# Kernel tuning notes

Hardware: AMD Instinct MI355X
Metric: run time of the kernel (lower is better)

## Reference

```python
import jax, jax.numpy as jnp
import numpy as np

N = 100000   # nodes
E = 1600000  # edges (before self-loops)
D_IN = 128
HID = 64
H1 = 4       # heads of conv1
OUT = 2
EPS = 1e-5
NEG_SLOPE = 0.2


def setup_inputs():
    key = jax.random.key(0)
    ks = jax.random.split(key, 12)
    s = 0.1
    return {
        "x": jax.random.normal(ks[0], (N, D_IN), jnp.float32),
        "edge_index": jax.random.randint(ks[1], (2, E), 0, N, jnp.int64),
        "W1": jax.random.normal(ks[2], (D_IN, H1 * HID), jnp.float32) * s,
        "att_src1": jax.random.normal(ks[3], (H1, HID), jnp.float32) * s,
        "att_dst1": jax.random.normal(ks[4], (H1, HID), jnp.float32) * s,
        "b1": jnp.zeros((H1 * HID,), jnp.float32),
        "g1": jnp.ones((H1 * HID,), jnp.float32),
        "be1": jnp.zeros((H1 * HID,), jnp.float32),
        "W2": jax.random.normal(ks[5], (H1 * HID, HID), jnp.float32) * s,
        "att_src2": jax.random.normal(ks[6], (1, HID), jnp.float32) * s,
        "att_dst2": jax.random.normal(ks[7], (1, HID), jnp.float32) * s,
        "b2": jnp.zeros((HID,), jnp.float32),
        "g2": jnp.ones((HID,), jnp.float32),
        "be2": jnp.zeros((HID,), jnp.float32),
        "Wc1": jax.random.normal(ks[8], (HID, HID // 2), jnp.float32) * s,
        "bc1": jnp.zeros((HID // 2,), jnp.float32),
        "Wc2": jax.random.normal(ks[9], (HID // 2, OUT), jnp.float32) * s,
        "bc2": jnp.zeros((OUT,), jnp.float32),
    }


def _gat(x, W, a_src, a_dst, bias, src, dst, heads):
    n = x.shape[0]
    h = (x @ W).reshape(n, heads, -1)              # [N,H,C]
    e_src = jnp.einsum('nhc,hc->nh', h, a_src)     # [N,H]
    e_dst = jnp.einsum('nhc,hc->nh', h, a_dst)
    e = jax.nn.leaky_relu(e_src[src] + e_dst[dst], NEG_SLOPE)  # [Etot,H]
    m = jax.ops.segment_max(e, dst, num_segments=n)            # edge-softmax over incoming
    p = jnp.exp(e - m[dst])
    z = jax.ops.segment_sum(p, dst, num_segments=n)
    alpha = p / z[dst]
    msg = alpha[:, :, None] * h[src]               # [Etot,H,C]
    out = jax.ops.segment_sum(msg, dst, num_segments=n)        # [N,H,C]
    return out.reshape(n, -1) + bias               # concat heads + bias


def _bn(x, g, b):
    m = x.mean(0)
    v = x.var(0)
    return g * (x - m) * jax.lax.rsqrt(v + EPS) + b


def reference(x, edge_index, W1, att_src1, att_dst1, b1, g1, be1,
              W2, att_src2, att_dst2, b2, g2, be2, Wc1, bc1, Wc2, bc2):
    n = x.shape[0]
    loops = jnp.arange(n, dtype=edge_index.dtype)
    src = jnp.concatenate([edge_index[0], loops])  # PyG add_self_loops=True
    dst = jnp.concatenate([edge_index[1], loops])

    h = _gat(x, W1, att_src1, att_dst1, b1, src, dst, H1)
    h = jax.nn.elu(_bn(h, g1, be1))                # dropout = identity (eval)
    h = _gat(h, W2, att_src2, att_dst2, b2, src, dst, 1)
    h = jax.nn.elu(_bn(h, g2, be2))
    h = jax.nn.elu(h @ Wc1 + bc1)
    logits = h @ Wc2 + bc2
    return jax.nn.log_softmax(logits, axis=1)
```

## Files before the change

kernel.cpp:

```cpp
#include <hip/hip_runtime.h>
#include <hip/hip_bf16.h>

constexpr int N_  = 100000;
constexpr int E_  = 1600000;
constexpr int PAD = 48;
constexpr int NBKT = 196;
constexpr int BCAP = 16384;

constexpr size_t P_PARAMS = 12288;
constexpr size_t OFF_WPK1 = 224000;
constexpr size_t OFF_WPK2 = 289536;
constexpr size_t OFF_DEG  = 322304;
constexpr size_t OFF_ES1  = 722304;
constexpr size_t OFF_ED1  = 2322304;
constexpr size_t OFF_ES2  = 3922304;
constexpr size_t OFF_ED2  = 4322304;
constexpr size_t OFF_CSR  = 4722304;
constexpr size_t OFF_H1   = 23922304;
constexpr size_t OFF_H2   = OFF_H1;
constexpr size_t OFF_AGG2 = OFF_H1 + 12800000;
constexpr size_t OFF_AGG1 = 75122304;
constexpr size_t OFF_BKT  = 126322304;

typedef unsigned short ushortT;
typedef short bf16x8 __attribute__((ext_vector_type(8)));
typedef float f32x4 __attribute__((ext_vector_type(4)));

#define DEV __device__ __forceinline__

DEV float leakyf(float x) { return x > 0.f ? x : 0.2f * x; }
DEV float eluf(float x)   { return x > 0.f ? x : __expf(x) - 1.f; }
DEV float rbf(unsigned short u) { unsigned int b = ((unsigned int)u) << 16; return __uint_as_float(b); }
DEV unsigned short f2b(float f) { __hip_bfloat16 h = __float2bfloat16(f); return *reinterpret_cast<unsigned short*>(&h); }
DEV float sel_head(float4 a, int hd) {
    float r = a.x;
    r = (hd == 1) ? a.y : r;
    r = (hd == 2) ? a.z : r;
    r = (hd == 3) ? a.w : r;
    return r;
}
DEV unsigned short sel_h4(ushort4 u, int hd) {
    unsigned short r = u.x;
    r = (hd == 1) ? u.y : r;
    r = (hd == 2) ? u.z : r;
    r = (hd == 3) ? u.w : r;
    return r;
}
DEV int eread(const int* __restrict__ ei, int mode, int idx) {
    return mode ? ei[(size_t)idx * 2] : ei[idx];
}

__global__ void k_detect2(const int* __restrict__ ei, const unsigned int* __restrict__ g1raw,
                          int* __restrict__ mode, int* __restrict__ fmode) {
    __shared__ int any;
    if (threadIdx.x == 0) any = 0;
    __syncthreads();
    if (ei[2 * threadIdx.x + 1] != 0) atomicOr(&any, 1);
    __syncthreads();
    if (threadIdx.x == 0) {
        *mode = any ? 0 : 1;
        *fmode = (g1raw[0] == 0x3F800000u) ? 0 : 1;
    }
}

struct CvtArgs { const void* src[16]; int off[17]; };
__global__ __launch_bounds__(256) void k_cvtall(CvtArgs a, float* __restrict__ dst,
                                                const int* __restrict__ fmode, int total) {
    int i = blockIdx.x * 256 + threadIdx.x;
    if (i >= total) return;
    int seg = 0;
    #pragma unroll
    for (int s2 = 1; s2 < 16; ++s2) seg += (i >= a.off[s2]);
    int j = i - a.off[seg];
    float v;
    if (*fmode) v = rbf(((const unsigned short*)a.src[seg])[j]);
    else        v = ((const float*)a.src[seg])[j];
    dst[i] = v;
}

__global__ __launch_bounds__(256) void k_packw(const float* __restrict__ pp,
                                               ushortT* __restrict__ w1, ushortT* __restrict__ w2) {
    int i = blockIdx.x * 256 + threadIdx.x;
    if (i < 32768) {
        int j = i & 7, lane = (i >> 3) & 63, ks = (i >> 9) & 3, ct = i >> 11;
        int src = (ks * 32 + ((lane >> 4) << 3) + j) * 256 + ct * 16 + (lane & 15);
        w1[i] = f2b(pp[src]);
    } else if (i < 49152) {
        int i2 = i - 32768;
        int j = i2 & 7, lane = (i2 >> 3) & 63, ks = (i2 >> 9) & 7, ct = i2 >> 12;
        int src = (ks * 32 + ((lane >> 4) << 3) + j) * 64 + ct * 16 + (lane & 15);
        w2[i2] = f2b(pp[34048 + src]);
    }
}

__global__ __launch_bounds__(256) void k_bin(const int* __restrict__ ei, const int* __restrict__ mode,
                                             unsigned int* __restrict__ bucketArr,
                                             int* __restrict__ bucketCursor) {
    __shared__ unsigned int pk[8192];
    __shared__ int cnt[256], scn[256], bse[256], cur[256], gb[256];
    int tid = threadIdx.x;
    cnt[tid] = 0;
    __syncthreads();
    int e0 = blockIdx.x * 8192;
    int m = *mode;
    #pragma unroll 4
    for (int j = 0; j < 32; ++j) {
        int e = e0 + j * 256 + tid;
        if (e < E_) atomicAdd(&cnt[eread(ei, m, E_ + e) >> 9], 1);
    }
    __syncthreads();
    int v = cnt[tid];
    scn[tid] = v;
    __syncthreads();
    for (int d = 1; d < 256; d <<= 1) {
        int t2 = (tid >= d) ? scn[tid - d] : 0;
        __syncthreads();
        scn[tid] += t2;
        __syncthreads();
    }
    int excl = scn[tid] - v;
    bse[tid] = excl;
    cur[tid] = excl;
    __syncthreads();
    #pragma unroll 4
    for (int j = 0; j < 32; ++j) {
        int e = e0 + j * 256 + tid;
        if (e < E_) {
            int s = eread(ei, m, e);
            int d = eread(ei, m, E_ + e);
            int b = d >> 9;
            int p = atomicAdd(&cur[b], 1);
            pk[p] = ((unsigned int)(d & 511) << 17) | (unsigned int)s;
        }
    }
    __syncthreads();
    if (tid < NBKT) {
        int c = cnt[tid];
        gb[tid] = (c > 0) ? atomicAdd(&bucketCursor[tid], c) : 0;
    }
    __syncthreads();
    int wv = tid >> 6, ln = tid & 63;
    for (int b = wv; b < NBKT; b += 4) {
        int c = cnt[b];
        int lo = bse[b], g = gb[b];
        for (int i = ln; i < c; i += 64) {
            int gi = g + i;
            if (gi < BCAP) bucketArr[(size_t)b * BCAP + gi] = pk[lo + i];
        }
    }
}

__global__ __launch_bounds__(256) void k_csr(const unsigned int* __restrict__ bucketArr,
                                             const int* __restrict__ bucketCursor,
                                             int* __restrict__ csr, int* __restrict__ deg) {
    __shared__ int dl[512];
    int tid = threadIdx.x;
    int b = blockIdx.x;
    int nbase = b * 512;
    int nb = min(N_ - nbase, 512);
    if (nb <= 0) return;
    dl[tid] = 0; dl[tid + 256] = 0;
    __syncthreads();
    int c = min(bucketCursor[b], BCAP);
    const unsigned int* run = bucketArr + (size_t)b * BCAP;
    for (int i = tid; i < c; i += 256) {
        unsigned int p = run[i];
        int s = (int)(p & 0x1FFFFu);
        int dloc = (int)(p >> 17);
        int slot = atomicAdd(&dl[dloc], 1);
        if (slot < PAD - 1) csr[(size_t)(nbase + dloc) * PAD + slot] = s;
    }
    __syncthreads();
    for (int t = tid; t < nb; t += 256) {
        int n = nbase + t;
        int cd = min(dl[t], PAD - 1);
        csr[(size_t)n * PAD + cd] = n;
        deg[n] = cd + 1;
    }
}

__global__ __launch_bounds__(256) void k_gemm1f(const void* __restrict__ x, const int* __restrict__ fmode,
                                                const ushortT* __restrict__ wpk,
                                                const float* __restrict__ as1, const float* __restrict__ ad1,
                                                ushortT* __restrict__ h1,
                                                float* __restrict__ es1, float* __restrict__ ed1) {
    __shared__ ushortT xs[32][132];
    int tid = threadIdx.x, w = tid >> 6, lane = tid & 63;
    int l15 = lane & 15, l4 = lane >> 4;
    int row0 = blockIdx.x * 32;
    if (*fmode) {
        const ushortT* xg = (const ushortT*)x + (size_t)row0 * 128;
        for (int i = tid; i < 512; i += 256) {
            int r = i >> 4, cc = (i & 15) * 8;
            ushort4 a = *(const ushort4*)(xg + r * 128 + cc);
            ushort4 b = *(const ushort4*)(xg + r * 128 + cc + 4);
            *(ushort4*)&xs[r][cc]     = a;
            *(ushort4*)&xs[r][cc + 4] = b;
        }
    } else {
        const float* xg = (const float*)x + (size_t)row0 * 128;
        for (int i = tid; i < 512; i += 256) {
            int r = i >> 4, cc = (i & 15) * 8;
            float4 a = *(const float4*)(xg + r * 128 + cc);
            float4 b = *(const float4*)(xg + r * 128 + cc + 4);
            *(ushort4*)&xs[r][cc]     = make_ushort4(f2b(a.x), f2b(a.y), f2b(a.z), f2b(a.w));
            *(ushort4*)&xs[r][cc + 4] = make_ushort4(f2b(b.x), f2b(b.y), f2b(b.z), f2b(b.w));
        }
    }
    __syncthreads();
    bf16x8 A[2][4];
    #pragma unroll
    for (int rt = 0; rt < 2; ++rt)
        #pragma unroll
        for (int ks = 0; ks < 4; ++ks)
            A[rt][ks] = *(const bf16x8*)&xs[rt * 16 + l15][ks * 32 + l4 * 8];
    f32x4 acc[2][4];
    #pragma unroll
    for (int rt = 0; rt < 2; ++rt)
        #pragma unroll
        for (int ct = 0; ct < 4; ++ct) acc[rt][ct] = (f32x4){0.f, 0.f, 0.f, 0.f};
    const bf16x8* wp = (const bf16x8*)wpk;
    #pragma unroll
    for (int ct = 0; ct < 4; ++ct) {
        int ctg = w * 4 + ct;
        bf16x8 B0 = wp[(ctg * 4 + 0) * 64 + lane];
        bf16x8 B1 = wp[(ctg * 4 + 1) * 64 + lane];
        bf16x8 B2 = wp[(ctg * 4 + 2) * 64 + lane];
        bf16x8 B3 = wp[(ctg * 4 + 3) * 64 + lane];
        #pragma unroll
        for (int rt = 0; rt < 2; ++rt) {
            acc[rt][ct] = __builtin_amdgcn_mfma_f32_16x16x32_bf16(A[rt][0], B0, acc[rt][ct], 0, 0, 0);
            acc[rt][ct] = __builtin_amdgcn_mfma_f32_16x16x32_bf16(A[rt][1], B1, acc[rt][ct], 0, 0, 0);
            acc[rt][ct] = __builtin_amdgcn_mfma_f32_16x16x32_bf16(A[rt][2], B2, acc[rt][ct], 0, 0, 0);
            acc[rt][ct] = __builtin_amdgcn_mfma_f32_16x16x32_bf16(A[rt][3], B3, acc[rt][ct], 0, 0, 0);
        }
    }
    float asc[4], adc[4];
    #pragma unroll
    for (int ct = 0; ct < 4; ++ct) {
        asc[ct] = as1[w * 64 + ct * 16 + l15];
        adc[ct] = ad1[w * 64 + ct * 16 + l15];
    }
    float pes[2][4], ped[2][4];
    #pragma unroll
    for (int rt = 0; rt < 2; ++rt)
        #pragma unroll
        for (int r = 0; r < 4; ++r) { pes[rt][r] = 0.f; ped[rt][r] = 0.f; }
    #pragma unroll
    for (int rt = 0; rt < 2; ++rt)
        #pragma unroll
        for (int ct = 0; ct < 4; ++ct)
            #pragma unroll
            for (int r = 0; r < 4; ++r) {
                float v = acc[rt][ct][r];
                int row = row0 + rt * 16 + l4 * 4 + r;
                h1[(size_t)row * 256 + w * 64 + ct * 16 + l15] = f2b(v);
                pes[rt][r] = fmaf(v, asc[ct], pes[rt][r]);
                ped[rt][r] = fmaf(v, adc[ct], ped[rt][r]);
            }
    #pragma unroll
    for (int d = 1; d < 16; d <<= 1)
        #pragma unroll
        for (int rt = 0; rt < 2; ++rt)
            #pragma unroll
            for (int r = 0; r < 4; ++r) {
                pes[rt][r] += __shfl_xor(pes[rt][r], d);
                ped[rt][r] += __shfl_xor(ped[rt][r], d);
            }
    if (l15 == 0) {
        #pragma unroll
        for (int rt = 0; rt < 2; ++rt)
            #pragma unroll
            for (int r = 0; r < 4; ++r) {
                int row = row0 + rt * 16 + l4 * 4 + r;
                es1[row * 4 + w] = pes[rt][r];
                ed1[row * 4 + w] = ped[rt][r];
            }
    }
}

__global__ __launch_bounds__(256) void k_lagg1(const ushortT* __restrict__ h1,
                                               const float* __restrict__ es1, const float* __restrict__ ed1,
                                               const int* __restrict__ deg, const int* __restrict__ csr,
                                               const float* __restrict__ b1, ushortT* __restrict__ out) {
    __shared__ int ssrc[4][PAD];
    __shared__ ushort4 sp[4][PAD];
    int wid = threadIdx.x >> 6;
    int lane = threadIdx.x & 63;
    int n = blockIdx.x * 4 + wid;
    int cnt = deg[n];
    int start = n * PAD;
    float4 ed = ((const float4*)ed1)[n];
    float z0 = 0.f, z1 = 0.f, z2 = 0.f, z3 = 0.f;
    if (lane < cnt) {
        int s = csr[start + lane];
        ssrc[wid][lane] = s;
        float4 es = ((const float4*)es1)[s];
        float p0 = __expf(leakyf(es.x + ed.x));
        float p1 = __expf(leakyf(es.y + ed.y));
        float p2 = __expf(leakyf(es.z + ed.z));
        float p3 = __expf(leakyf(es.w + ed.w));
        sp[wid][lane] = make_ushort4(f2b(p0), f2b(p1), f2b(p2), f2b(p3));
        z0 = p0; z1 = p1; z2 = p2; z3 = p3;
    }
    #pragma unroll
    for (int d = 1; d < 64; d <<= 1) {
        z0 += __shfl_xor(z0, d); z1 += __shfl_xor(z1, d);
        z2 += __shfl_xor(z2, d); z3 += __shfl_xor(z3, d);
    }
    int half = lane >> 5, lh = lane & 31, hd = lh >> 3;
    float izh = sel_head(make_float4(1.f / z0, 1.f / z1, 1.f / z2, 1.f / z3), hd);
    float a0 = 0.f, a1 = 0.f, a2 = 0.f, a3 = 0.f, a4 = 0.f, a5 = 0.f, a6 = 0.f, a7 = 0.f;
    float c0 = 0.f, c1 = 0.f, c2 = 0.f, c3 = 0.f, c4 = 0.f, c5 = 0.f, c6 = 0.f, c7 = 0.f;
    int iters = (cnt + 1) >> 1;
    for (int t = 0; t < iters; t += 4) {
        int i0 = 2 * t + half;
        int i1 = i0 + 2, i2 = i0 + 4, i3 = i0 + 6;
        bool v0 = i0 < cnt, v1 = i1 < cnt, v2 = i2 < cnt, v3 = i3 < cnt;
        int s0 = ssrc[wid][v0 ? i0 : 0];
        int s1 = ssrc[wid][v1 ? i1 : 0];
        int s2 = ssrc[wid][v2 ? i2 : 0];
        int s3 = ssrc[wid][v3 ? i3 : 0];
        ushort4 u0 = sp[wid][v0 ? i0 : 0];
        ushort4 u1 = sp[wid][v1 ? i1 : 0];
        ushort4 u2 = sp[wid][v2 ? i2 : 0];
        ushort4 u3 = sp[wid][v3 ? i3 : 0];
        float w0 = v0 ? rbf(sel_h4(u0, hd)) * izh : 0.f;
        float w1 = v1 ? rbf(sel_h4(u1, hd)) * izh : 0.f;
        float w2 = v2 ? rbf(sel_h4(u2, hd)) * izh : 0.f;
        float w3 = v3 ? rbf(sel_h4(u3, hd)) * izh : 0.f;
        uint4 r0 = *(const uint4*)(h1 + (size_t)s0 * 256 + lh * 8);
        uint4 r1 = *(const uint4*)(h1 + (size_t)s1 * 256 + lh * 8);
        uint4 r2 = *(const uint4*)(h1 + (size_t)s2 * 256 + lh * 8);
        uint4 r3 = *(const uint4*)(h1 + (size_t)s3 * 256 + lh * 8);
        a0 = fmaf(w0, rbf((unsigned short)(r0.x & 0xffff)), a0);
        a1 = fmaf(w0, rbf((unsigned short)(r0.x >> 16)), a1);
        a2 = fmaf(w0, rbf((unsigned short)(r0.y & 0xffff)), a2);
        a3 = fmaf(w0, rbf((unsigned short)(r0.y >> 16)), a3);
        a4 = fmaf(w0, rbf((unsigned short)(r0.z & 0xffff)), a4);
        a5 = fmaf(w0, rbf((unsigned short)(r0.z >> 16)), a5);
        a6 = fmaf(w0, rbf((unsigned short)(r0.w & 0xffff)), a6);
        a7 = fmaf(w0, rbf((unsigned short)(r0.w >> 16)), a7);
        c0 = fmaf(w1, rbf((unsigned short)(r1.x & 0xffff)), c0);
        c1 = fmaf(w1, rbf((unsigned short)(r1.x >> 16)), c1);
        c2 = fmaf(w1, rbf((unsigned short)(r1.y & 0xffff)), c2);
        c3 = fmaf(w1, rbf((unsigned short)(r1.y >> 16)), c3);
        c4 = fmaf(w1, rbf((unsigned short)(r1.z & 0xffff)), c4);
        c5 = fmaf(w1, rbf((unsigned short)(r1.z >> 16)), c5);
        c6 = fmaf(w1, rbf((unsigned short)(r1.w & 0xffff)), c6);
        c7 = fmaf(w1, rbf((unsigned short)(r1.w >> 16)), c7);
        a0 = fmaf(w2, rbf((unsigned short)(r2.x & 0xffff)), a0);
        a1 = fmaf(w2, rbf((unsigned short)(r2.x >> 16)), a1);
        a2 = fmaf(w2, rbf((unsigned short)(r2.y & 0xffff)), a2);
        a3 = fmaf(w2, rbf((unsigned short)(r2.y >> 16)), a3);
        a4 = fmaf(w2, rbf((unsigned short)(r2.z & 0xffff)), a4);
        a5 = fmaf(w2, rbf((unsigned short)(r2.z >> 16)), a5);
        a6 = fmaf(w2, rbf((unsigned short)(r2.w & 0xffff)), a6);
        a7 = fmaf(w2, rbf((unsigned short)(r2.w >> 16)), a7);
        c0 = fmaf(w3, rbf((unsigned short)(r3.x & 0xffff)), c0);
        c1 = fmaf(w3, rbf((unsigned short)(r3.x >> 16)), c1);
        c2 = fmaf(w3, rbf((unsigned short)(r3.y & 0xffff)), c2);
        c3 = fmaf(w3, rbf((unsigned short)(r3.y >> 16)), c3);
        c4 = fmaf(w3, rbf((unsigned short)(r3.z & 0xffff)), c4);
        c5 = fmaf(w3, rbf((unsigned short)(r3.z >> 16)), c5);
        c6 = fmaf(w3, rbf((unsigned short)(r3.w & 0xffff)), c6);
        c7 = fmaf(w3, rbf((unsigned short)(r3.w >> 16)), c7);
    }
    a0 += c0; a1 += c1; a2 += c2; a3 += c3; a4 += c4; a5 += c5; a6 += c6; a7 += c7;
    a0 += __shfl_xor(a0, 32); a1 += __shfl_xor(a1, 32);
    a2 += __shfl_xor(a2, 32); a3 += __shfl_xor(a3, 32);
    a4 += __shfl_xor(a4, 32); a5 += __shfl_xor(a5, 32);
    a6 += __shfl_xor(a6, 32); a7 += __shfl_xor(a7, 32);
    if (half == 0) {
        float4 b0 = *(const float4*)(b1 + lh * 8);
        float4 b1v = *(const float4*)(b1 + lh * 8 + 4);
        ushort4 o0 = make_ushort4(f2b(a0 + b0.x), f2b(a1 + b0.y), f2b(a2 + b0.z), f2b(a3 + b0.w));
        ushort4 o1 = make_ushort4(f2b(a4 + b1v.x), f2b(a5 + b1v.y), f2b(a6 + b1v.z), f2b(a7 + b1v.w));
        *(ushort4*)(out + (size_t)n * 256 + lh * 8)     = o0;
        *(ushort4*)(out + (size_t)n * 256 + lh * 8 + 4) = o1;
    }
}

__global__ __launch_bounds__(256) void k_bnstats1(const ushortT* __restrict__ a, double* __restrict__ sums,
                                                  double* __restrict__ sumsq) {
    int c = threadIdx.x;
    int r0 = blockIdx.x * 256;
    int r1 = min(r0 + 256, N_);
    double s = 0.0, q = 0.0;
    for (int r = r0; r < r1; ++r) { float v = rbf(a[(size_t)r * 256 + c]); s += v; q += (double)v * v; }
    atomicAdd(&sums[c], s);
    atomicAdd(&sumsq[c], q);
}

__global__ void k_bnfin(const double* __restrict__ sums, const double* __restrict__ sumsq,
                        const float* __restrict__ g, const float* __restrict__ be,
                        float* __restrict__ s, float* __restrict__ t, int C) {
    int c = threadIdx.x;
    if (c < C) {
        double mean = sums[c] / (double)N_;
        double var = fmax(sumsq[c] / (double)N_ - mean * mean, 0.0);
        double sc = (double)g[c] / sqrt(var + 1e-5);
        s[c] = (float)sc;
        t[c] = (float)((double)be[c] - mean * sc);
    }
}

__global__ __launch_bounds__(256) void k_gemm2f(const ushortT* __restrict__ agg1,
                                                const ushortT* __restrict__ wpk2,
                                                const float* __restrict__ sc1, const float* __restrict__ tc1,
                                                const float* __restrict__ as2, const float* __restrict__ ad2,
                                                ushortT* __restrict__ h2,
                                                float* __restrict__ es2, float* __restrict__ ed2) {
    int tid = threadIdx.x, w = tid >> 6, lane = tid & 63;
    int l15 = lane & 15, l4 = lane >> 4;
    int row0 = blockIdx.x * 64;
    int arow = row0 + w * 16 + l15;
    int ar = min(arow, N_ - 1);
    bf16x8 A[8];
    #pragma unroll
    for (int ks = 0; ks < 8; ++ks) {
        const ushortT* ap = agg1 + (size_t)ar * 256 + ks * 32 + l4 * 8;
        int pi = ks * 32 + l4 * 8;
        uint4 u = *(const uint4*)ap;
        float4 s0 = *(const float4*)(sc1 + pi);
        float4 s1 = *(const float4*)(sc1 + pi + 4);
        float4 t0 = *(const float4*)(tc1 + pi);
        float4 t1 = *(const float4*)(tc1 + pi + 4);
        float e0 = eluf(fmaf(rbf((unsigned short)(u.x & 0xffff)), s0.x, t0.x));
        float e1 = eluf(fmaf(rbf((unsigned short)(u.x >> 16)),    s0.y, t0.y));
        float e2 = eluf(fmaf(rbf((unsigned short)(u.y & 0xffff)), s0.z, t0.z));
        float e3 = eluf(fmaf(rbf((unsigned short)(u.y >> 16)),    s0.w, t0.w));
        float e4 = eluf(fmaf(rbf((unsigned short)(u.z & 0xffff)), s1.x, t1.x));
        float e5 = eluf(fmaf(rbf((unsigned short)(u.z >> 16)),    s1.y, t1.y));
        float e6 = eluf(fmaf(rbf((unsigned short)(u.w & 0xffff)), s1.z, t1.z));
        float e7 = eluf(fmaf(rbf((unsigned short)(u.w >> 16)),    s1.w, t1.w));
        A[ks] = (bf16x8){(short)f2b(e0), (short)f2b(e1), (short)f2b(e2), (short)f2b(e3),
                         (short)f2b(e4), (short)f2b(e5), (short)f2b(e6), (short)f2b(e7)};
    }
    f32x4 acc[4];
    #pragma unroll
    for (int ct = 0; ct < 4; ++ct) acc[ct] = (f32x4){0.f, 0.f, 0.f, 0.f};
    const bf16x8* wp = (const bf16x8*)wpk2;
    #pragma unroll
    for (int ct = 0; ct < 4; ++ct) {
        #pragma unroll
        for (int ks = 0; ks < 8; ++ks) {
            bf16x8 B = wp[(ct * 8 + ks) * 64 + lane];
            acc[ct] = __builtin_amdgcn_mfma_f32_16x16x32_bf16(A[ks], B, acc[ct], 0, 0, 0);
        }
    }
    float asc[4], adc[4];
    #pragma unroll
    for (int ct = 0; ct < 4; ++ct) {
        asc[ct] = as2[ct * 16 + l15];
        adc[ct] = ad2[ct * 16 + l15];
    }
    float pes[4] = {0.f, 0.f, 0.f, 0.f}, ped[4] = {0.f, 0.f, 0.f, 0.f};
    #pragma unroll
    for (int ct = 0; ct < 4; ++ct)
        #pragma unroll
        for (int r = 0; r < 4; ++r) {
            float v = acc[ct][r];
            int row = row0 + w * 16 + l4 * 4 + r;
            if (row < N_) h2[(size_t)row * 64 + ct * 16 + l15] = f2b(v);
            pes[r] = fmaf(v, asc[ct], pes[r]);
            ped[r] = fmaf(v, adc[ct], ped[r]);
        }
    #pragma unroll
    for (int d = 1; d < 16; d <<= 1)
        #pragma unroll
        for (int r = 0; r < 4; ++r) {
            pes[r] += __shfl_xor(pes[r], d);
            ped[r] += __shfl_xor(ped[r], d);
        }
    if (l15 == 0) {
        #pragma unroll
        for (int r = 0; r < 4; ++r) {
            int row = row0 + w * 16 + l4 * 4 + r;
            if (row < N_) { es2[row] = pes[r]; ed2[row] = ped[r]; }
        }
    }
}

__global__ __launch_bounds__(256) void k_lagg2(const ushortT* __restrict__ h2,
                                               const float* __restrict__ es2, const float* __restrict__ ed2,
                                               const int* __restrict__ deg, const int* __restrict__ csr,
                                               const float* __restrict__ b2, float* __restrict__ out) {
    __shared__ int ssrc[4][PAD];
    __shared__ float sp[4][PAD];
    int wid = threadIdx.x >> 6;
    int lane = threadIdx.x & 63;
    int n = blockIdx.x * 4 + wid;
    int cnt = deg[n];
    int start = n * PAD;
    float ed = ed2[n];
    float z = 0.f;
    if (lane < cnt) {
        int s = csr[start + lane];
        ssrc[wid][lane] = s;
        float p = __expf(leakyf(es2[s] + ed));
        sp[wid][lane] = p;
        z = p;
    }
    #pragma unroll
    for (int d = 1; d < 64; d <<= 1) z += __shfl_xor(z, d);
    float iz = 1.f / z;
    int half = lane >> 5, lh = lane & 31;
    float a0 = 0.f, a1 = 0.f, c0 = 0.f, c1 = 0.f;
    int iters = (cnt + 1) >> 1;
    for (int t = 0; t < iters; t += 4) {
        int i0 = 2 * t + half;
        int i1 = i0 + 2, i2 = i0 + 4, i3 = i0 + 6;
        bool v0 = i0 < cnt, v1 = i1 < cnt, v2 = i2 < cnt, v3 = i3 < cnt;
        int s0 = ssrc[wid][v0 ? i0 : 0];
        int s1 = ssrc[wid][v1 ? i1 : 0];
        int s2 = ssrc[wid][v2 ? i2 : 0];
        int s3 = ssrc[wid][v3 ? i3 : 0];
        float w0 = v0 ? sp[wid][i0] * iz : 0.f;
        float w1 = v1 ? sp[wid][i1] * iz : 0.f;
        float w2 = v2 ? sp[wid][i2] * iz : 0.f;
        float w3 = v3 ? sp[wid][i3] * iz : 0.f;
        unsigned int u0 = *(const unsigned int*)(h2 + (size_t)s0 * 64 + lh * 2);
        unsigned int u1 = *(const unsigned int*)(h2 + (size_t)s1 * 64 + lh * 2);
        unsigned int u2 = *(const unsigned int*)(h2 + (size_t)s2 * 64 + lh * 2);
        unsigned int u3 = *(const unsigned int*)(h2 + (size_t)s3 * 64 + lh * 2);
        a0 = fmaf(w0, rbf((unsigned short)(u0 & 0xffff)), a0);
        a1 = fmaf(w0, rbf((unsigned short)(u0 >> 16)), a1);
        c0 = fmaf(w1, rbf((unsigned short)(u1 & 0xffff)), c0);
        c1 = fmaf(w1, rbf((unsigned short)(u1 >> 16)), c1);
        a0 = fmaf(w2, rbf((unsigned short)(u2 & 0xffff)), a0);
        a1 = fmaf(w2, rbf((unsigned short)(u2 >> 16)), a1);
        c0 = fmaf(w3, rbf((unsigned short)(u3 & 0xffff)), c0);
        c1 = fmaf(w3, rbf((unsigned short)(u3 >> 16)), c1);
    }
    a0 += c0; a1 += c1;
    a0 += __shfl_xor(a0, 32);
    a1 += __shfl_xor(a1, 32);
    if (half == 0) {
        out[(size_t)n * 64 + lh * 2 + 0] = a0 + b2[lh * 2 + 0];
        out[(size_t)n * 64 + lh * 2 + 1] = a1 + b2[lh * 2 + 1];
    }
}

__global__ __launch_bounds__(256) void k_bnstats2(const float* __restrict__ a, double* __restrict__ sums,
                                                  double* __restrict__ sumsq) {
    __shared__ double sm[256], sq[256];
    int tid = threadIdx.x;
    int c = tid & 63, rr = tid >> 6;
    int r0 = blockIdx.x * 1024;
    int r1 = min(r0 + 1024, N_);
    double s = 0.0, q = 0.0;
    for (int r = r0 + rr; r < r1; r += 4) { float v = a[(size_t)r * 64 + c]; s += v; q += (double)v * v; }
    sm[tid] = s; sq[tid] = q; __syncthreads();
    if (tid < 64) {
        s = sm[tid] + sm[tid + 64] + sm[tid + 128] + sm[tid + 192];
        q = sq[tid] + sq[tid + 64] + sq[tid + 128] + sq[tid + 192];
        atomicAdd(&sums[tid], s);
        atomicAdd(&sumsq[tid], q);
    }
}

__global__ __launch_bounds__(256) void k_cls(const float* __restrict__ agg2, const float* __restrict__ Wc1,
                                             const float* __restrict__ bc1, const float* __restrict__ Wc2,
                                             const float* __restrict__ bc2, const float* __restrict__ s2,
                                             const float* __restrict__ t2, float* __restrict__ out) {
    __shared__ float w1s[2048];
    __shared__ float w2s[64];
    __shared__ float b1s[32];
    __shared__ float b2s[2];
    __shared__ float ss[64], ts[64];
    int tid = threadIdx.x;
    for (int i = tid; i < 2048; i += 256) w1s[i] = Wc1[i];
    if (tid < 64) { w2s[tid] = Wc2[tid]; ss[tid] = s2[tid]; ts[tid] = t2[tid]; }
    if (tid < 32) b1s[tid] = bc1[tid];
    if (tid < 2)  b2s[tid] = bc2[tid];
    __syncthreads();
    int n = blockIdx.x * 256 + tid;
    if (n >= N_) return;
    float hv[64];
    const float4* rp = (const float4*)(agg2 + (size_t)n * 64);
    #pragma unroll
    for (int q = 0; q < 16; ++q) {
        float4 v = rp[q];
        float tmp[4] = {v.x, v.y, v.z, v.w};
        #pragma unroll
        for (int c4 = 0; c4 < 4; ++c4) {
            int c = q * 4 + c4;
            hv[c] = eluf(fmaf(tmp[c4], ss[c], ts[c]));
        }
    }
    float l0 = b2s[0], l1 = b2s[1];
    for (int j = 0; j < 32; ++j) {
        float a = b1s[j];
        #pragma unroll
        for (int k = 0; k < 64; ++k) a = fmaf(hv[k], w1s[k * 32 + j], a);
        float u = eluf(a);
        l0 = fmaf(u, w2s[j * 2 + 0], l0);
        l1 = fmaf(u, w2s[j * 2 + 1], l1);
    }
    float mx = fmaxf(l0, l1);
    float lse = mx + __logf(__expf(l0 - mx) + __expf(l1 - mx));
    out[(size_t)n * 2 + 0] = l0 - lse;
    out[(size_t)n * 2 + 1] = l1 - lse;
}

extern "C" void kernel_launch(void* const* d_in, const int* in_sizes, int n_in,
                              void* d_out, int out_size, void* d_ws, size_t ws_size,
                              hipStream_t stream) {
    float* out = (float*)d_out;

    char* ws = (char*)d_ws;
    double* sums1  = (double*)(ws + 0);
    double* sumsq1 = (double*)(ws + 2048);
    double* sums2  = (double*)(ws + 4096);
    double* sumsq2 = (double*)(ws + 4608);
    int* bcur = (int*)(ws + 5120);
    float* s1 = (float*)(ws + 6144), *t1 = (float*)(ws + 7168);
    float* s2 = (float*)(ws + 8192), *t2 = (float*)(ws + 8448);
    int* mode  = (int*)(ws + 8704);
    int* fmode = (int*)(ws + 8708);

    float* pp   = (float*)(ws + P_PARAMS);
    float* as1f = pp + 32768;
    float* ad1f = pp + 33024;
    float* b1f  = pp + 33280;
    float* g1f  = pp + 33536;
    float* be1f = pp + 33792;
    float* as2f = pp + 50432;
    float* ad2f = pp + 50496;
    float* b2f  = pp + 50560;
    float* g2f  = pp + 50624;
    float* be2f = pp + 50688;
    float* Wc1f = pp + 50752;
    float* bc1f = pp + 52800;
    float* Wc2f = pp + 52832;
    float* bc2f = pp + 52896;
    const int CV_TOTAL = 52898;

    ushortT* wpk1 = (ushortT*)(ws + OFF_WPK1);
    ushortT* wpk2 = (ushortT*)(ws + OFF_WPK2);
    int* deg    = (int*)(ws + OFF_DEG);
    int* csr    = (int*)(ws + OFF_CSR);
    float* es1  = (float*)(ws + OFF_ES1);
    float* ed1  = (float*)(ws + OFF_ED1);
    float* es2  = (float*)(ws + OFF_ES2);
    float* ed2  = (float*)(ws + OFF_ED2);
    ushortT* h1 = (ushortT*)(ws + OFF_H1);
    ushortT* h2 = (ushortT*)(ws + OFF_H2);
    float* agg2 = (float*)(ws + OFF_AGG2);
    ushortT* agg1 = (ushortT*)(ws + OFF_AGG1);
    unsigned int* bkt = (unsigned int*)(ws + OFF_BKT);

    hipMemsetAsync(ws, 0, 6144, stream);
    k_detect2<<<1, 256, 0, stream>>>((const int*)d_in[1], (const unsigned int*)d_in[6], mode, fmode);

    CvtArgs ca;
    const int srcIdx[16] = {2,3,4,5,6,7,8,9,10,11,12,13,14,15,16,17};
    const int offsEl[17] = {0,32768,33024,33280,33536,33792,34048,50432,50496,50560,
                            50624,50688,50752,52800,52832,52896,52898};
    for (int i = 0; i < 16; ++i) ca.src[i] = d_in[srcIdx[i]];
    for (int i = 0; i < 17; ++i) ca.off[i] = offsEl[i];
    k_cvtall<<<(CV_TOTAL + 255) / 256, 256, 0, stream>>>(ca, pp, fmode, CV_TOTAL);
    k_packw <<<192, 256, 0, stream>>>(pp, wpk1, wpk2);

    k_bin<<<(E_ + 8191) / 8192, 256, 0, stream>>>((const int*)d_in[1], mode, bkt, bcur);
    k_csr<<<NBKT, 256, 0, stream>>>(bkt, bcur, csr, deg);

    k_gemm1f<<<N_ / 32, 256, 0, stream>>>(d_in[0], fmode, wpk1, as1f, ad1f, h1, es1, ed1);
    k_lagg1<<<N_ / 4, 256, 0, stream>>>(h1, es1, ed1, deg, csr, b1f, agg1);
    k_bnstats1<<<(N_ + 255) / 256, 256, 0, stream>>>(agg1, sums1, sumsq1);
    k_bnfin<<<1, 256, 0, stream>>>(sums1, sumsq1, g1f, be1f, s1, t1, 256);

    k_gemm2f<<<(N_ + 63) / 64, 256, 0, stream>>>(agg1, wpk2, s1, t1, as2f, ad2f, h2, es2, ed2);
    k_lagg2<<<N_ / 4, 256, 0, stream>>>(h2, es2, ed2, deg, csr, b2f, agg2);
    k_bnstats2<<<98, 256, 0, stream>>>(agg2, sums2, sumsq2);
    k_bnfin<<<1, 64, 0, stream>>>(sums2, sumsq2, g2f, be2f, s2, t2, 64);

    k_cls<<<(N_ + 255) / 256, 256, 0, stream>>>(agg2, Wc1f, bc1f, Wc2f, bc2f, s2, t2, out);
}
```

Baseline: 473.3 us.

## Fuse setup kernels, cache edges in LDS, unroll gathers, vectorize BN stats

Merges the detect, convert and weight-pack setup kernels into one kernel that reads raw weights directly, and folds the edge-format detection into the binning kernel. k_bin now keeps src/dst in shared memory so it does not reread edges from global memory. Both aggregation loops issue eight gathers before doing the FMAs, giving more memory-level parallelism. BN stats for layer 1 use 16-byte loads, float partial sums and a shared-memory reduction. The risks are more LDS per bin block, which lowers occupancy, and float rather than double accumulation inside each block.

```diff
diff --git a/kernel.cpp b/kernel.cpp
--- a/kernel.cpp
+++ b/kernel.cpp
@@ -7,20 +7,24 @@
 constexpr int NBKT = 196;
 constexpr int BCAP = 16384;
 
-constexpr size_t P_PARAMS = 12288;
-constexpr size_t OFF_WPK1 = 224000;
-constexpr size_t OFF_WPK2 = 289536;
-constexpr size_t OFF_DEG  = 322304;
-constexpr size_t OFF_ES1  = 722304;
-constexpr size_t OFF_ED1  = 2322304;
-constexpr size_t OFF_ES2  = 3922304;
-constexpr size_t OFF_ED2  = 4322304;
-constexpr size_t OFF_CSR  = 4722304;
-constexpr size_t OFF_H1   = 23922304;
+constexpr size_t P_PARAMS = 8192;
+constexpr size_t OFF_S1   = 24576;
+constexpr size_t OFF_T1   = 25600;
+constexpr size_t OFF_S2   = 26624;
+constexpr size_t OFF_T2   = 26880;
+constexpr size_t OFF_WPK1 = 27136;
+constexpr size_t OFF_WPK2 = 92672;
+constexpr size_t OFF_DEG  = 125696;
+constexpr size_t OFF_ES1  = 525696;
+constexpr size_t OFF_ED1  = 2125696;
+constexpr size_t OFF_ES2  = 3725696;
+constexpr size_t OFF_ED2  = 4125696;
+constexpr size_t OFF_CSR  = 4525696;
+constexpr size_t OFF_H1   = 23725696;
 constexpr size_t OFF_H2   = OFF_H1;
 constexpr size_t OFF_AGG2 = OFF_H1 + 12800000;
-constexpr size_t OFF_AGG1 = 75122304;
-constexpr size_t OFF_BKT  = 126322304;
+constexpr size_t OFF_AGG1 = 74925696;
+constexpr size_t OFF_BKT  = 126125696;
 
 typedef unsigned short ushortT;
 typedef short bf16x8 __attribute__((ext_vector_type(8)));
@@ -49,64 +53,66 @@
 DEV int eread(const int* __restrict__ ei, int mode, int idx) {
     return mode ? ei[(size_t)idx * 2] : ei[idx];
 }
-
-__global__ void k_detect2(const int* __restrict__ ei, const unsigned int* __restrict__ g1raw,
-                          int* __restrict__ mode, int* __restrict__ fmode) {
-    __shared__ int any;
-    if (threadIdx.x == 0) any = 0;
-    __syncthreads();
-    if (ei[2 * threadIdx.x + 1] != 0) atomicOr(&any, 1);
-    __syncthreads();
-    if (threadIdx.x == 0) {
-        *mode = any ? 0 : 1;
-        *fmode = (g1raw[0] == 0x3F800000u) ? 0 : 1;
-    }
-}
-
-struct CvtArgs { const void* src[16]; int off[17]; };
-__global__ __launch_bounds__(256) void k_cvtall(CvtArgs a, float* __restrict__ dst,
-                                                const int* __restrict__ fmode, int total) {
+DEV unsigned short praw(const void* p, int fm, int idx) {
+    return fm ? ((const ushortT*)p)[idx] : f2b(((const float*)p)[idx]);
+}
+
+struct CvtArgs { const void* src[14]; int off[15]; };
+__global__ __launch_bounds__(256) void k_setup(const void* __restrict__ W1raw, const void* __restrict__ W2raw,
+                                               const unsigned int* __restrict__ g1raw, CvtArgs ca,
+                                               ushortT* __restrict__ w1, ushortT* __restrict__ w2,
+                                               float* __restrict__ pp) {
     int i = blockIdx.x * 256 + threadIdx.x;
-    if (i >= total) return;
-    int seg = 0;
-    #pragma unroll
-    for (int s2 = 1; s2 < 16; ++s2) seg += (i >= a.off[s2]);
-    int j = i - a.off[seg];
-    float v;
-    if (*fmode) v = rbf(((const unsigned short*)a.src[seg])[j]);
-    else        v = ((const float*)a.src[seg])[j];
-    dst[i] = v;
-}
-
-__global__ __launch_bounds__(256) void k_packw(const float* __restrict__ pp,
-                                               ushortT* __restrict__ w1, ushortT* __restrict__ w2) {
-    int i = blockIdx.x * 256 + threadIdx.x;
+    int fm = (g1raw[0] == 0x3F800000u) ? 0 : 1;
     if (i < 32768) {
         int j = i & 7, lane = (i >> 3) & 63, ks = (i >> 9) & 3, ct = i >> 11;
         int src = (ks * 32 + ((lane >> 4) << 3) + j) * 256 + ct * 16 + (lane & 15);
-        w1[i] = f2b(pp[src]);
+        w1[i] = praw(W1raw, fm, src);
     } else if (i < 49152) {
         int i2 = i - 32768;
         int j = i2 & 7, lane = (i2 >> 3) & 63, ks = (i2 >> 9) & 7, ct = i2 >> 12;
         int src = (ks * 32 + ((lane >> 4) << 3) + j) * 64 + ct * 16 + (lane & 15);
-        w2[i2] = f2b(pp[34048 + src]);
-    }
-}
-
-__global__ __launch_bounds__(256) void k_bin(const int* __restrict__ ei, const int* __restrict__ mode,
+        w2[i2] = praw(W2raw, fm, src);
+    } else if (i < 52898) {
+        int j = i - 49152;
+        int seg = 0;
+        #pragma unroll
+        for (int s2 = 1; s2 < 14; ++s2) seg += (j >= ca.off[s2]);
+        int k = j - ca.off[seg];
+        float v;
+        if (fm) v = rbf(((const ushortT*)ca.src[seg])[k]);
+        else    v = ((const float*)ca.src[seg])[k];
+        pp[j] = v;
+    }
+}
+
+__global__ __launch_bounds__(256) void k_bin(const int* __restrict__ ei,
                                              unsigned int* __restrict__ bucketArr,
                                              int* __restrict__ bucketCursor) {
     __shared__ unsigned int pk[8192];
+    __shared__ int sdl[8192];
+    __shared__ int ssl[8192];
     __shared__ int cnt[256], scn[256], bse[256], cur[256], gb[256];
+    __shared__ int any;
     int tid = threadIdx.x;
     cnt[tid] = 0;
-    __syncthreads();
+    if (tid == 0) any = 0;
+    __syncthreads();
+    if (ei[2 * tid + 1] != 0) atomicOr(&any, 1);
+    __syncthreads();
+    int m = any ? 0 : 1;
     int e0 = blockIdx.x * 8192;
-    int m = *mode;
     #pragma unroll 4
     for (int j = 0; j < 32; ++j) {
-        int e = e0 + j * 256 + tid;
-        if (e < E_) atomicAdd(&cnt[eread(ei, m, E_ + e) >> 9], 1);
+        int idx = j * 256 + tid;
+        int e = e0 + idx;
+        if (e < E_) {
+            int s = eread(ei, m, e);
+            int d = eread(ei, m, E_ + e);
+            ssl[idx] = s;
+            sdl[idx] = d;
+            atomicAdd(&cnt[d >> 9], 1);
+        }
     }
     __syncthreads();
     int v = cnt[tid];
@@ -124,10 +130,10 @@
     __syncthreads();
     #pragma unroll 4
     for (int j = 0; j < 32; ++j) {
-        int e = e0 + j * 256 + tid;
+        int idx = j * 256 + tid;
+        int e = e0 + idx;
         if (e < E_) {
-            int s = eread(ei, m, e);
-            int d = eread(ei, m, E_ + e);
+            int s = ssl[idx], d = sdl[idx];
             int b = d >> 9;
             int p = atomicAdd(&cur[b], 1);
             pk[p] = ((unsigned int)(d & 511) << 17) | (unsigned int)s;
@@ -179,7 +185,8 @@
     }
 }
 
-__global__ __launch_bounds__(256) void k_gemm1f(const void* __restrict__ x, const int* __restrict__ fmode,
+__global__ __launch_bounds__(256) void k_gemm1f(const void* __restrict__ x,
+                                                const unsigned int* __restrict__ g1raw,
                                                 const ushortT* __restrict__ wpk,
                                                 const float* __restrict__ as1, const float* __restrict__ ad1,
                                                 ushortT* __restrict__ h1,
@@ -188,7 +195,8 @@
     int tid = threadIdx.x, w = tid >> 6, lane = tid & 63;
     int l15 = lane & 15, l4 = lane >> 4;
     int row0 = blockIdx.x * 32;
-    if (*fmode) {
+    int fm = (g1raw[0] == 0x3F800000u) ? 0 : 1;
+    if (fm) {
         const ushortT* xg = (const ushortT*)x + (size_t)row0 * 128;
         for (int i = tid; i < 512; i += 256) {
             int r = i >> 4, cc = (i & 15) * 8;
@@ -313,58 +321,43 @@
     float a0 = 0.f, a1 = 0.f, a2 = 0.f, a3 = 0.f, a4 = 0.f, a5 = 0.f, a6 = 0.f, a7 = 0.f;
     float c0 = 0.f, c1 = 0.f, c2 = 0.f, c3 = 0.f, c4 = 0.f, c5 = 0.f, c6 = 0.f, c7 = 0.f;
     int iters = (cnt + 1) >> 1;
-    for (int t = 0; t < iters; t += 4) {
-        int i0 = 2 * t + half;
-        int i1 = i0 + 2, i2 = i0 + 4, i3 = i0 + 6;
-        bool v0 = i0 < cnt, v1 = i1 < cnt, v2 = i2 < cnt, v3 = i3 < cnt;
-        int s0 = ssrc[wid][v0 ? i0 : 0];
-        int s1 = ssrc[wid][v1 ? i1 : 0];
-        int s2 = ssrc[wid][v2 ? i2 : 0];
-        int s3 = ssrc[wid][v3 ? i3 : 0];
-        ushort4 u0 = sp[wid][v0 ? i0 : 0];
-        ushort4 u1 = sp[wid][v1 ? i1 : 0];
-        ushort4 u2 = sp[wid][v2 ? i2 : 0];
-        ushort4 u3 = sp[wid][v3 ? i3 : 0];
-        float w0 = v0 ? rbf(sel_h4(u0, hd)) * izh : 0.f;
-        float w1 = v1 ? rbf(sel_h4(u1, hd)) * izh : 0.f;
-        float w2 = v2 ? rbf(sel_h4(u2, hd)) * izh : 0.f;
-        float w3 = v3 ? rbf(sel_h4(u3, hd)) * izh : 0.f;
-        uint4 r0 = *(const uint4*)(h1 + (size_t)s0 * 256 + lh * 8);
-        uint4 r1 = *(const uint4*)(h1 + (size_t)s1 * 256 + lh * 8);
-        uint4 r2 = *(const uint4*)(h1 + (size_t)s2 * 256 + lh * 8);
-        uint4 r3 = *(const uint4*)(h1 + (size_t)s3 * 256 + lh * 8);
-        a0 = fmaf(w0, rbf((unsigned short)(r0.x & 0xffff)), a0);
-        a1 = fmaf(w0, rbf((unsigned short)(r0.x >> 16)), a1);
-        a2 = fmaf(w0, rbf((unsigned short)(r0.y & 0xffff)), a2);
-        a3 = fmaf(w0, rbf((unsigned short)(r0.y >> 16)), a3);
-        a4 = fmaf(w0, rbf((unsigned short)(r0.z & 0xffff)), a4);
-        a5 = fmaf(w0, rbf((unsigned short)(r0.z >> 16)), a5);
-        a6 = fmaf(w0, rbf((unsigned short)(r0.w & 0xffff)), a6);
-        a7 = fmaf(w0, rbf((unsigned short)(r0.w >> 16)), a7);
-        c0 = fmaf(w1, rbf((unsigned short)(r1.x & 0xffff)), c0);
-        c1 = fmaf(w1, rbf((unsigned short)(r1.x >> 16)), c1);
-        c2 = fmaf(w1, rbf((unsigned short)(r1.y & 0xffff)), c2);
-        c3 = fmaf(w1, rbf((unsigned short)(r1.y >> 16)), c3);
-        c4 = fmaf(w1, rbf((unsigned short)(r1.z & 0xffff)), c4);
-        c5 = fmaf(w1, rbf((unsigned short)(r1.z >> 16)), c5);
-        c6 = fmaf(w1, rbf((unsigned short)(r1.w & 0xffff)), c6);
-        c7 = fmaf(w1, rbf((unsigned short)(r1.w >> 16)), c7);
-        a0 = fmaf(w2, rbf((unsigned short)(r2.x & 0xffff)), a0);
-        a1 = fmaf(w2, rbf((unsigned short)(r2.x >> 16)), a1);
-        a2 = fmaf(w2, rbf((unsigned short)(r2.y & 0xffff)), a2);
-        a3 = fmaf(w2, rbf((unsigned short)(r2.y >> 16)), a3);
-        a4 = fmaf(w2, rbf((unsigned short)(r2.z & 0xffff)), a4);
-        a5 = fmaf(w2, rbf((unsigned short)(r2.z >> 16)), a5);
-        a6 = fmaf(w2, rbf((unsigned short)(r2.w & 0xffff)), a6);
-        a7 = fmaf(w2, rbf((unsigned short)(r2.w >> 16)), a7);
-        c0 = fmaf(w3, rbf((unsigned short)(r3.x & 0xffff)), c0);
-        c1 = fmaf(w3, rbf((unsigned short)(r3.x >> 16)), c1);
-        c2 = fmaf(w3, rbf((unsigned short)(r3.y & 0xffff)), c2);
-        c3 = fmaf(w3, rbf((unsigned short)(r3.y >> 16)), c3);
-        c4 = fmaf(w3, rbf((unsigned short)(r3.z & 0xffff)), c4);
-        c5 = fmaf(w3, rbf((unsigned short)(r3.z >> 16)), c5);
-        c6 = fmaf(w3, rbf((unsigned short)(r3.w & 0xffff)), c6);
-        c7 = fmaf(w3, rbf((unsigned short)(r3.w >> 16)), c7);
+    for (int t = 0; t < iters; t += 8) {
+        int sArr[8]; float wArr[8]; uint4 rArr[8];
+        #pragma unroll
+        for (int u = 0; u < 8; ++u) {
+            int i = 2 * (t + u) + half;
+            bool v = i < cnt;
+            sArr[u] = ssrc[wid][v ? i : 0];
+            ushort4 uu = sp[wid][v ? i : 0];
+            wArr[u] = v ? rbf(sel_h4(uu, hd)) * izh : 0.f;
+        }
+        #pragma unroll
+        for (int u = 0; u < 8; ++u)
+            rArr[u] = *(const uint4*)(h1 + (size_t)sArr[u] * 256 + lh * 8);
+        #pragma unroll
+        for (int u = 0; u < 8; ++u) {
+            float wv = wArr[u];
+            uint4 r = rArr[u];
+            if (u & 1) {
+                c0 = fmaf(wv, rbf((unsigned short)(r.x & 0xffff)), c0);
+                c1 = fmaf(wv, rbf((unsigned short)(r.x >> 16)), c1);
+                c2 = fmaf(wv, rbf((unsigned short)(r.y & 0xffff)), c2);
+                c3 = fmaf(wv, rbf((unsigned short)(r.y >> 16)), c3);
+                c4 = fmaf(wv, rbf((unsigned short)(r.z & 0xffff)), c4);
+                c5 = fmaf(wv, rbf((unsigned short)(r.z >> 16)), c5);
+                c6 = fmaf(wv, rbf((unsigned short)(r.w & 0xffff)), c6);
+                c7 = fmaf(wv, rbf((unsigned short)(r.w >> 16)), c7);
+            } else {
+                a0 = fmaf(wv, rbf((unsigned short)(r.x & 0xffff)), a0);
+                a1 = fmaf(wv, rbf((unsigned short)(r.x >> 16)), a1);
+                a2 = fmaf(wv, rbf((unsigned short)(r.y & 0xffff)), a2);
+                a3 = fmaf(wv, rbf((unsigned short)(r.y >> 16)), a3);
+                a4 = fmaf(wv, rbf((unsigned short)(r.z & 0xffff)), a4);
+                a5 = fmaf(wv, rbf((unsigned short)(r.z >> 16)), a5);
+                a6 = fmaf(wv, rbf((unsigned short)(r.w & 0xffff)), a6);
+                a7 = fmaf(wv, rbf((unsigned short)(r.w >> 16)), a7);
+            }
+        }
     }
     a0 += c0; a1 += c1; a2 += c2; a3 += c3; a4 += c4; a5 += c5; a6 += c6; a7 += c7;
     a0 += __shfl_xor(a0, 32); a1 += __shfl_xor(a1, 32);
@@ -383,13 +376,38 @@
 
 __global__ __launch_bounds__(256) void k_bnstats1(const ushortT* __restrict__ a, double* __restrict__ sums,
                                                   double* __restrict__ sumsq) {
-    int c = threadIdx.x;
-    int r0 = blockIdx.x * 256;
-    int r1 = min(r0 + 256, N_);
-    double s = 0.0, q = 0.0;
-    for (int r = r0; r < r1; ++r) { float v = rbf(a[(size_t)r * 256 + c]); s += v; q += (double)v * v; }
-    atomicAdd(&sums[c], s);
-    atomicAdd(&sumsq[c], q);
+    __shared__ float lss[256][9], lsq[256][9];
+    int tid = threadIdx.x;
+    int c8 = tid & 31, rr = tid >> 5;
+    int r0 = blockIdx.x * 512;
+    int r1 = min(r0 + 512, N_);
+    float s[8] = {0, 0, 0, 0, 0, 0, 0, 0}, q[8] = {0, 0, 0, 0, 0, 0, 0, 0};
+    for (int r = r0 + rr; r < r1; r += 8) {
+        uint4 u = *(const uint4*)(a + (size_t)r * 256 + c8 * 8);
+        unsigned int uw[4] = {u.x, u.y, u.z, u.w};
+        #pragma unroll
+        for (int k = 0; k < 4; ++k) {
+            float v0 = rbf((unsigned short)(uw[k] & 0xffff));
+            float v1 = rbf((unsigned short)(uw[k] >> 16));
+            s[2 * k]     += v0; q[2 * k]     += v0 * v0;
+            s[2 * k + 1] += v1; q[2 * k + 1] += v1 * v1;
+        }
+    }
+    #pragma unroll
+    for (int k = 0; k < 8; ++k) { lss[tid][k] = s[k]; lsq[tid][k] = q[k]; }
+    __syncthreads();
+    if (tid < 32) {
+        float S[8] = {0, 0, 0, 0, 0, 0, 0, 0}, Q[8] = {0, 0, 0, 0, 0, 0, 0, 0};
+        #pragma unroll
+        for (int g = 0; g < 8; ++g)
+            #pragma unroll
+            for (int k = 0; k < 8; ++k) { S[k] += lss[g * 32 + tid][k]; Q[k] += lsq[g * 32 + tid][k]; }
+        #pragma unroll
+        for (int k = 0; k < 8; ++k) {
+            atomicAdd(&sums[tid * 8 + k], (double)S[k]);
+            atomicAdd(&sumsq[tid * 8 + k], (double)Q[k]);
+        }
+    }
 }
 
 __global__ void k_bnfin(const double* __restrict__ sums, const double* __restrict__ sumsq,
@@ -508,30 +526,30 @@
     int half = lane >> 5, lh = lane & 31;
     float a0 = 0.f, a1 = 0.f, c0 = 0.f, c1 = 0.f;
     int iters = (cnt + 1) >> 1;
-    for (int t = 0; t < iters; t += 4) {
-        int i0 = 2 * t + half;
-        int i1 = i0 + 2, i2 = i0 + 4, i3 = i0 + 6;
-        bool v0 = i0 < cnt, v1 = i1 < cnt, v2 = i2 < cnt, v3 = i3 < cnt;
-        int s0 = ssrc[wid][v0 ? i0 : 0];
-        int s1 = ssrc[wid][v1 ? i1 : 0];
-        int s2 = ssrc[wid][v2 ? i2 : 0];
-        int s3 = ssrc[wid][v3 ? i3 : 0];
-        float w0 = v0 ? sp[wid][i0] * iz : 0.f;
-        float w1 = v1 ? sp[wid][i1] * iz : 0.f;
-        float w2 = v2 ? sp[wid][i2] * iz : 0.f;
-        float w3 = v3 ? sp[wid][i3] * iz : 0.f;
-        unsigned int u0 = *(const unsigned int*)(h2 + (size_t)s0 * 64 + lh * 2);
-        unsigned int u1 = *(const unsigned int*)(h2 + (size_t)s1 * 64 + lh * 2);
-        unsigned int u2 = *(const unsigned int*)(h2 + (size_t)s2 * 64 + lh * 2);
-        unsigned int u3 = *(const unsigned int*)(h2 + (size_t)s3 * 64 + lh * 2);
-        a0 = fmaf(w0, rbf((unsigned short)(u0 & 0xffff)), a0);
-        a1 = fmaf(w0, rbf((unsigned short)(u0 >> 16)), a1);
-        c0 = fmaf(w1, rbf((unsigned short)(u1 & 0xffff)), c0);
-        c1 = fmaf(w1, rbf((unsigned short)(u1 >> 16)), c1);
-        a0 = fmaf(w2, rbf((unsigned short)(u2 & 0xffff)), a0);
-        a1 = fmaf(w2, rbf((unsigned short)(u2 >> 16)), a1);
-        c0 = fmaf(w3, rbf((unsigned short)(u3 & 0xffff)), c0);
-        c1 = fmaf(w3, rbf((unsigned short)(u3 >> 16)), c1);
+    for (int t = 0; t < iters; t += 8) {
+        int sArr[8]; float wArr[8]; unsigned int uArr[8];
+        #pragma unroll
+        for (int u = 0; u < 8; ++u) {
+            int i = 2 * (t + u) + half;
+            bool v = i < cnt;
+            sArr[u] = ssrc[wid][v ? i : 0];
+            wArr[u] = v ? sp[wid][v ? i : 0] * iz : 0.f;
+        }
+        #pragma unroll
+        for (int u = 0; u < 8; ++u)
+            uArr[u] = *(const unsigned int*)(h2 + (size_t)sArr[u] * 64 + lh * 2);
+        #pragma unroll
+        for (int u = 0; u < 8; ++u) {
+            float wv = wArr[u];
+            unsigned int uu = uArr[u];
+            if (u & 1) {
+                c0 = fmaf(wv, rbf((unsigned short)(uu & 0xffff)), c0);
+                c1 = fmaf(wv, rbf((unsigned short)(uu >> 16)), c1);
+            } else {
+                a0 = fmaf(wv, rbf((unsigned short)(uu & 0xffff)), a0);
+                a1 = fmaf(wv, rbf((unsigned short)(uu >> 16)), a1);
+            }
+        }
     }
     a0 += c0; a1 += c1;
     a0 += __shfl_xor(a0, 32);
@@ -615,27 +633,24 @@
     double* sums2  = (double*)(ws + 4096);
     double* sumsq2 = (double*)(ws + 4608);
     int* bcur = (int*)(ws + 5120);
-    float* s1 = (float*)(ws + 6144), *t1 = (float*)(ws + 7168);
-    float* s2 = (float*)(ws + 8192), *t2 = (float*)(ws + 8448);
-    int* mode  = (int*)(ws + 8704);
-    int* fmode = (int*)(ws + 8708);
+    float* s1 = (float*)(ws + OFF_S1), *t1 = (float*)(ws + OFF_T1);
+    float* s2 = (float*)(ws + OFF_S2), *t2 = (float*)(ws + OFF_T2);
 
     float* pp   = (float*)(ws + P_PARAMS);
-    float* as1f = pp + 32768;
-    float* ad1f = pp + 33024;
-    float* b1f  = pp + 33280;
-    float* g1f  = pp + 33536;
-    float* be1f = pp + 33792;
-    float* as2f = pp + 50432;
-    float* ad2f = pp + 50496;
-    float* b2f  = pp + 50560;
-    float* g2f  = pp + 50624;
-    float* be2f = pp + 50688;
-    float* Wc1f = pp + 50752;
-    float* bc1f = pp + 52800;
-    float* Wc2f = pp + 52832;
-    float* bc2f = pp + 52896;
-    const int CV_TOTAL = 52898;
+    float* as1f = pp + 0;
+    float* ad1f = pp + 256;
+    float* b1f  = pp + 512;
+    float* g1f  = pp + 768;
+    float* be1f = pp + 1024;
+    float* as2f = pp + 1280;
+    float* ad2f = pp + 1344;
+    float* b2f  = pp + 1408;
+    float* g2f  = pp + 1472;
+    float* be2f = pp + 1536;
+    float* Wc1f = pp + 1600;
+    float* bc1f = pp + 3648;
+    float* Wc2f = pp + 3680;
+    float* bc2f = pp + 3744;
 
     ushortT* wpk1 = (ushortT*)(ws + OFF_WPK1);
     ushortT* wpk2 = (ushortT*)(ws + OFF_WPK2);
@@ -652,23 +667,20 @@
     unsigned int* bkt = (unsigned int*)(ws + OFF_BKT);
 
     hipMemsetAsync(ws, 0, 6144, stream);
-    k_detect2<<<1, 256, 0, stream>>>((const int*)d_in[1], (const unsigned int*)d_in[6], mode, fmode);
 
     CvtArgs ca;
-    const int srcIdx[16] = {2,3,4,5,6,7,8,9,10,11,12,13,14,15,16,17};
-    const int offsEl[17] = {0,32768,33024,33280,33536,33792,34048,50432,50496,50560,
-                            50624,50688,50752,52800,52832,52896,52898};
-    for (int i = 0; i < 16; ++i) ca.src[i] = d_in[srcIdx[i]];
-    for (int i = 0; i < 17; ++i) ca.off[i] = offsEl[i];
-    k_cvtall<<<(CV_TOTAL + 255) / 256, 256, 0, stream>>>(ca, pp, fmode, CV_TOTAL);
-    k_packw <<<192, 256, 0, stream>>>(pp, wpk1, wpk2);
-
-    k_bin<<<(E_ + 8191) / 8192, 256, 0, stream>>>((const int*)d_in[1], mode, bkt, bcur);
+    const int srcIdx[14] = {3, 4, 5, 6, 7, 9, 10, 11, 12, 13, 14, 15, 16, 17};
+    const int offsEl[15] = {0, 256, 512, 768, 1024, 1280, 1344, 1408, 1472, 1536, 1600, 3648, 3680, 3744, 3746};
+    for (int i = 0; i < 14; ++i) ca.src[i] = d_in[srcIdx[i]];
+    for (int i = 0; i < 15; ++i) ca.off[i] = offsEl[i];
+    k_setup<<<207, 256, 0, stream>>>(d_in[2], d_in[8], (const unsigned int*)d_in[6], ca, wpk1, wpk2, pp);
+
+    k_bin<<<(E_ + 8191) / 8192, 256, 0, stream>>>((const int*)d_in[1], bkt, bcur);
     k_csr<<<NBKT, 256, 0, stream>>>(bkt, bcur, csr, deg);
 
-    k_gemm1f<<<N_ / 32, 256, 0, stream>>>(d_in[0], fmode, wpk1, as1f, ad1f, h1, es1, ed1);
+    k_gemm1f<<<N_ / 32, 256, 0, stream>>>(d_in[0], (const unsigned int*)d_in[6], wpk1, as1f, ad1f, h1, es1, ed1);
     k_lagg1<<<N_ / 4, 256, 0, stream>>>(h1, es1, ed1, deg, csr, b1f, agg1);
-    k_bnstats1<<<(N_ + 255) / 256, 256, 0, stream>>>(agg1, sums1, sumsq1);
+    k_bnstats1<<<196, 256, 0, stream>>>(agg1, sums1, sumsq1);
     k_bnfin<<<1, 256, 0, stream>>>(sums1, sumsq1, g1f, be1f, s1, t1, 256);
 
     k_gemm2f<<<(N_ + 63) / 64, 256, 0, stream>>>(agg1, wpk2, s1, t1, as2f, ad2f, h2, es2, ed2);
```

Result: faster. 460.4 us (-2.7%).
